# Optimization experiments

Hardware: AMD Instinct MI355X
Metric: run time of the kernel (lower is better)

## Reference

```python
import jax, jax.numpy as jnp
import numpy as np


def _segment_sparsemax(x, batch, B):
    """Per-group sparsemax over a flat ragged tensor.

    x: [N] float values; batch: [N] sorted int group ids in [0, B).
    Groups are contiguous, so an in-group descending sort is a stable
    lexsort on (batch, -x); per-group cumsum is a global cumsum minus the
    cumsum value just before each group's start offset.
    """
    N = x.shape[0]
    num_nodes = jax.ops.segment_sum(jnp.ones(N, jnp.int32), batch, num_segments=B)  # [B]
    start = jnp.concatenate([jnp.zeros(1, jnp.int32), jnp.cumsum(num_nodes)[:-1]])  # [B]

    # shift by per-group max for numerical stability (as in torch forward)
    gmax = jax.ops.segment_max(x, batch, num_segments=B)
    xs = x - gmax[batch]

    # descending sort within each contiguous group
    order = jnp.lexsort((-xs, batch))
    sx = xs[order]  # [N], group-wise descending; group layout unchanged

    # per-group cumulative sum via global cumsum + start offsets
    cs = jnp.cumsum(sx)
    off = jnp.where(start > 0, cs[jnp.maximum(start - 1, 0)], jnp.zeros((), sx.dtype))  # [B]
    seg_cs = cs - off[batch] - 1.0  # input_cumsum - 1.0

    # rho = 1..n_g within each group
    rho = (jnp.arange(N, dtype=jnp.int32) - start[batch] + 1).astype(xs.dtype)

    support = rho * sx > seg_cs  # [N] bool
    supp_size = jax.ops.segment_sum(support.astype(jnp.int32), batch, num_segments=B)  # [B]

    idx = jnp.maximum(supp_size + start - 1, 0)  # [B]
    tau = seg_cs[idx] / supp_size.astype(xs.dtype)  # [B]

    return jnp.maximum(xs - tau[batch], 0.0)


def setup_inputs() -> dict:
    key = jax.random.key(0)
    k1, k2 = jax.random.split(key)
    N = 8_388_608
    B = 4096
    x = jax.random.normal(k1, (N,), dtype=jnp.float32)
    batch = jnp.sort(jax.random.randint(k2, (N,), 0, B)).astype(jnp.int64)
    return {"x": x, "batch": batch, "num_groups": B}


def reference(x, batch, num_groups):
    batch = batch.astype(jnp.int32)
    return _segment_sparsemax(x, batch, int(num_groups))
```

## Files before the change

### kernel.cpp

```cpp
#include <hip/hip_runtime.h>

#define BLK 256
#define QPT 3
#define CAPB (QPT * BLK * 4)
#define CCAP 320


__device__ __forceinline__ float wave_max(float v) {
#pragma unroll
  for (int o = 32; o; o >>= 1) v = fmaxf(v, __shfl_xor(v, o));
  return v;
}
__device__ __forceinline__ float wave_sum(float v) {
#pragma unroll
  for (int o = 32; o; o >>= 1) v += __shfl_xor(v, o);
  return v;
}
__device__ __forceinline__ int wave_sum_i(int v) {
#pragma unroll
  for (int o = 32; o; o >>= 1) v += __shfl_xor(v, o);
  return v;
}

__device__ __forceinline__ void block_sum_cnt(float& s, int& c, float* redf, int* redi, int tid) {
  s = wave_sum(s); c = wave_sum_i(c);
  __syncthreads();
  if ((tid & 63) == 0) { redf[tid >> 6] = s; redi[tid >> 6] = c; }
  __syncthreads();
  s = redf[0] + redf[1] + redf[2] + redf[3];
  c = redi[0] + redi[1] + redi[2] + redi[3];
}

__device__ __forceinline__ int wave_lower_bound(const int* __restrict__ batch, int N,
                                                int target, int lane) {
  int lo = 0, hi = N;
  while (hi > lo) {
    const long long span = hi - lo;
    const int m = lo + (int)((span * (long long)(lane + 1)) / 65);
    const int flag = (batch[m] < target) ? 1 : 0;
    const unsigned long long bal = __ballot(flag);
    const int c = __popcll(bal);
    int nlo = lo, nhi = hi;
    if (c > 0)  nlo = lo + (int)((span * (long long)c) / 65) + 1;
    if (c < 64) nhi = lo + (int)((span * (long long)(c + 1)) / 65);
    lo = nlo; hi = nhi;
  }
  return lo;
}


extern "C" __global__ void __launch_bounds__(BLK)
sparsemax_fused(const float* __restrict__ x, const int* __restrict__ batch,
                const int* __restrict__ pB, float* __restrict__ out, int N) {
  __shared__ float redf[4];
  __shared__ int   redi[4];
  __shared__ float cand[CCAP];
  __shared__ float sorted[64];
  __shared__ int   s_se[2];
  __shared__ int   s_cnt;
  __shared__ float s_csum;
  __shared__ float s_tau;
  const int tid  = threadIdx.x;
  const int lane = tid & 63;
  const int w    = tid >> 6;
  const int B = *pB;

  for (int g = blockIdx.x; g < B; g += gridDim.x) {
    if (w == 0) {
      const int v = wave_lower_bound(batch, N, g, lane);
      if (lane == 0) { s_se[0] = v; s_cnt = 0; s_csum = 0.0f; }
    } else if (w == 1) {
      const int v = wave_lower_bound(batch, N, g + 1, lane);
      if (lane == 0) s_se[1] = v;
    }
    __syncthreads();
    const int s = s_se[0];
    const int e = s_se[1];
    const int n = e - s;
    if (n <= 0) { __syncthreads(); continue; }
    const int a0 = s & ~3;

    if (e - a0 <= CAPB) {
      float4 r[QPT];
      float lmax = -INFINITY;
#pragma unroll
      for (int j = 0; j < QPT; ++j) {
        const int idx = a0 + (j * BLK + tid) * 4;
        float4 v = make_float4(-INFINITY, -INFINITY, -INFINITY, -INFINITY);
        if (idx < e) {
          if (idx + 4 <= N) {
            v = *(const float4*)(x + idx);
          } else {
            if (idx + 0 < N) v.x = x[idx + 0];
            if (idx + 1 < N) v.y = x[idx + 1];
            if (idx + 2 < N) v.z = x[idx + 2];
            if (idx + 3 < N) v.w = x[idx + 3];
          }
          if (idx + 0 < s || idx + 0 >= e) v.x = -INFINITY;
          if (idx + 1 < s || idx + 1 >= e) v.y = -INFINITY;
          if (idx + 2 < s || idx + 2 >= e) v.z = -INFINITY;
          if (idx + 3 < s || idx + 3 >= e) v.w = -INFINITY;
        }
        r[j] = v;
        lmax = fmaxf(lmax, fmaxf(fmaxf(v.x, v.y), fmaxf(v.z, v.w)));
      }
      lmax = wave_max(lmax);
      if (lane == 0) redf[w] = lmax;
      __syncthreads();
      const float gmax = fmaxf(fmaxf(redf[0], redf[1]), fmaxf(redf[2], redf[3]));
      const float thr = gmax - 1.0f;

      float wsum = 0.0f;
#pragma unroll
      for (int j = 0; j < QPT; ++j) {
        const float vv[4] = {r[j].x, r[j].y, r[j].z, r[j].w};
#pragma unroll
        for (int t = 0; t < 4; ++t) {
          const bool p = vv[t] > thr;
          const unsigned long long bal = __ballot(p);
          if (bal) {
            int base = 0;
            if (lane == 0) base = atomicAdd(&s_cnt, __popcll(bal));
            base = __shfl(base, 0);
            if (p) {
              const int off = base + __popcll(bal & ((1ull << lane) - 1ull));
              if (off < CCAP) cand[off] = vv[t];
              wsum += vv[t] - gmax;
            }
          }
        }
      }
      wsum = wave_sum(wsum);
      if (lane == 0) atomicAdd(&s_csum, wsum);
      __syncthreads();
      const int c = s_cnt;

      if (c <= 64) {
        if (w == 0) {
          const float v = (lane < c) ? cand[lane] - gmax : 0.0f;
          int rank = 0;
          for (int q = 0; q < c; ++q) {
            const float t = cand[q] - gmax;
            rank += (t > v) || (t == v && q < lane);
          }
          if (lane < c) sorted[rank] = v;
          const float sv = (lane < c) ? sorted[lane] : 0.0f;
          float cs = sv;
#pragma unroll
          for (int o = 1; o < 64; o <<= 1) {
            const float t2 = __shfl_up(cs, o);
            if (lane >= o) cs += t2;
          }
          const int flag = (lane < c) && (sv * (float)(lane + 1) > cs - 1.0f);
          const unsigned long long bal2 = __ballot(flag);
          const int k = 63 - __clzll(bal2);
          const float csk = __shfl(cs, k);
          if (lane == 0) s_tau = (csk - 1.0f) / (float)(k + 1);
        }
      } else if (c <= CCAP) {
        if (w == 0) {
          float tau = (s_csum - 1.0f) / (float)c;
          int cnt = c;
          for (int it = 0; it < 64; ++it) {
            float s2 = 0.0f; int c2 = 0;
            for (int q = lane; q < c; q += 64) {
              const float vs = cand[q] - gmax;
              if (vs > tau) { s2 += vs; c2++; }
            }
            s2 = wave_sum(s2); c2 = wave_sum_i(c2);
            if (c2 == cnt || c2 == 0) break;
            tau = (s2 - 1.0f) / (float)c2; cnt = c2;
          }
          if (lane == 0) s_tau = tau;
        }
      } else {
        float tau = (s_csum - 1.0f) / (float)c;
        int cnt = c;
        for (int it = 0; it < 64; ++it) {
          float s2 = 0.0f; int c2 = 0;
#pragma unroll
          for (int j = 0; j < QPT; ++j) {
            const float vv[4] = {r[j].x, r[j].y, r[j].z, r[j].w};
#pragma unroll
            for (int t = 0; t < 4; ++t) {
              const float vs = vv[t] - gmax;
              if (vs > tau) { s2 += vs; c2++; }
            }
          }
          block_sum_cnt(s2, c2, redf, redi, tid);
          if (c2 == cnt || c2 == 0) break;
          tau = (s2 - 1.0f) / (float)c2; cnt = c2;
        }
        if (tid == 0) s_tau = tau;
      }
      __syncthreads();
      const float sub = s_tau + gmax;

#pragma unroll
      for (int j = 0; j < QPT; ++j) {
        const int idx = a0 + (j * BLK + tid) * 4;
        if (idx >= e) continue;
        if (idx >= s && idx + 4 <= e) {
          float4 o4;
          o4.x = fmaxf(r[j].x - sub, 0.0f);
          o4.y = fmaxf(r[j].y - sub, 0.0f);
          o4.z = fmaxf(r[j].z - sub, 0.0f);
          o4.w = fmaxf(r[j].w - sub, 0.0f);
          *(float4*)(out + idx) = o4;
        } else {
          const float vv[4] = {r[j].x, r[j].y, r[j].z, r[j].w};
#pragma unroll
          for (int t = 0; t < 4; ++t) {
            const int p2 = idx + t;
            if (p2 >= s && p2 < e) out[p2] = fmaxf(vv[t] - sub, 0.0f);
          }
        }
      }
    } else {
      float gmax = -INFINITY;
      for (int i = s + tid; i < e; i += BLK) gmax = fmaxf(gmax, x[i]);
      gmax = wave_max(gmax);
      if (lane == 0) redf[w] = gmax;
      __syncthreads();
      gmax = fmaxf(fmaxf(redf[0], redf[1]), fmaxf(redf[2], redf[3]));
      float bs = 0.0f; int bc = 0;
      for (int i = s + tid; i < e; i += BLK) {
        const float vs = x[i] - gmax;
        if (vs > -1.0f) { bs += vs; bc++; }
      }
      block_sum_cnt(bs, bc, redf, redi, tid);
      float tau = (bs - 1.0f) / (float)bc;
      int cntS = bc;
      for (int it = 0; it < 64; ++it) {
        float s2 = 0.0f; int c2 = 0;
        for (int i = s + tid; i < e; i += BLK) {
          const float vs = x[i] - gmax;
          if (vs > tau) { s2 += vs; c2++; }
        }
        block_sum_cnt(s2, c2, redf, redi, tid);
        if (c2 == cntS || c2 == 0) break;
        tau = (s2 - 1.0f) / (float)c2; cntS = c2;
      }
      const float sub = tau + gmax;
      for (int i = s + tid; i < e; i += BLK) out[i] = fmaxf(x[i] - sub, 0.0f);
    }
    __syncthreads();
  }
}

extern "C" void kernel_launch(void* const* d_in, const int* in_sizes, int n_in,
                              void* d_out, int out_size, void* d_ws, size_t ws_size,
                              hipStream_t stream) {
  const float* x     = (const float*)d_in[0];
  const int*   batch = (const int*)d_in[1];
  const int*   pB    = (const int*)d_in[2];
  float*       out   = (float*)d_out;
  const int N = in_sizes[0];

  sparsemax_fused<<<dim3(4096), dim3(BLK), 0, stream>>>(x, batch, pB, out, N);
}
```

Measured before the change: 116.0 us.

## Split group boundary search into separate kernel and compact candidates per wave

Moves the per-group binary search over batch ids into a prior kernel that writes a starts array to workspace, so each group block reads its bounds directly instead of running two wave-wide searches followed by a barrier. It also adds a fast path for fully interior float4 loads. Candidate compaction now uses a per-lane count and a wave prefix scan with one atomic per wave, replacing twelve ballot/atomic rounds. The cost is an extra kernel launch and a workspace round trip, and the trailing barrier at the end of each group iteration is removed.

```diff
diff --git a/kernel.cpp b/kernel.cpp
--- a/kernel.cpp
+++ b/kernel.cpp
@@ -50,13 +50,29 @@
 
 
 extern "C" __global__ void __launch_bounds__(BLK)
-sparsemax_fused(const float* __restrict__ x, const int* __restrict__ batch,
-                const int* __restrict__ pB, float* __restrict__ out, int N) {
+build_starts_bs(const int* __restrict__ batch, int* __restrict__ starts,
+                const int* __restrict__ pB, int N) {
+  const int B = *pB;
+  const int lane = threadIdx.x & 63;
+  const int w    = threadIdx.x >> 6;
+  const int wpg  = gridDim.x * (BLK / 64);
+  for (int t = blockIdx.x * (BLK / 64) + w; t <= B; t += wpg) {
+    int v;
+    if (t == 0) v = 0;
+    else if (t >= B) v = N;
+    else v = wave_lower_bound(batch, N, t, lane);
+    if (lane == 0) starts[t] = v;
+  }
+}
+
+
+extern "C" __global__ void __launch_bounds__(BLK)
+sparsemax_groups(const float* __restrict__ x, const int* __restrict__ starts,
+                 const int* __restrict__ pB, float* __restrict__ out, int N) {
   __shared__ float redf[4];
   __shared__ int   redi[4];
   __shared__ float cand[CCAP];
   __shared__ float sorted[64];
-  __shared__ int   s_se[2];
   __shared__ int   s_cnt;
   __shared__ float s_csum;
   __shared__ float s_tau;
@@ -66,18 +82,10 @@
   const int B = *pB;
 
   for (int g = blockIdx.x; g < B; g += gridDim.x) {
-    if (w == 0) {
-      const int v = wave_lower_bound(batch, N, g, lane);
-      if (lane == 0) { s_se[0] = v; s_cnt = 0; s_csum = 0.0f; }
-    } else if (w == 1) {
-      const int v = wave_lower_bound(batch, N, g + 1, lane);
-      if (lane == 0) s_se[1] = v;
-    }
-    __syncthreads();
-    const int s = s_se[0];
-    const int e = s_se[1];
+    const int s = starts[g];
+    const int e = starts[g + 1];
     const int n = e - s;
-    if (n <= 0) { __syncthreads(); continue; }
+    if (n <= 0) continue;
     const int a0 = s & ~3;
 
     if (e - a0 <= CAPB) {
@@ -86,48 +94,61 @@
 #pragma unroll
       for (int j = 0; j < QPT; ++j) {
         const int idx = a0 + (j * BLK + tid) * 4;
-        float4 v = make_float4(-INFINITY, -INFINITY, -INFINITY, -INFINITY);
-        if (idx < e) {
-          if (idx + 4 <= N) {
-            v = *(const float4*)(x + idx);
-          } else {
-            if (idx + 0 < N) v.x = x[idx + 0];
-            if (idx + 1 < N) v.y = x[idx + 1];
-            if (idx + 2 < N) v.z = x[idx + 2];
-            if (idx + 3 < N) v.w = x[idx + 3];
-          }
-          if (idx + 0 < s || idx + 0 >= e) v.x = -INFINITY;
-          if (idx + 1 < s || idx + 1 >= e) v.y = -INFINITY;
-          if (idx + 2 < s || idx + 2 >= e) v.z = -INFINITY;
-          if (idx + 3 < s || idx + 3 >= e) v.w = -INFINITY;
+        float4 v;
+        if (idx >= s && idx + 4 <= e) {
+          v = *(const float4*)(x + idx);
+        } else {
+          v = make_float4(-INFINITY, -INFINITY, -INFINITY, -INFINITY);
+          if (idx < e) {
+            if (idx + 4 <= N) {
+              v = *(const float4*)(x + idx);
+            } else {
+              if (idx + 0 < N) v.x = x[idx + 0];
+              if (idx + 1 < N) v.y = x[idx + 1];
+              if (idx + 2 < N) v.z = x[idx + 2];
+              if (idx + 3 < N) v.w = x[idx + 3];
+            }
+            if (idx + 0 < s || idx + 0 >= e) v.x = -INFINITY;
+            if (idx + 1 < s || idx + 1 >= e) v.y = -INFINITY;
+            if (idx + 2 < s || idx + 2 >= e) v.z = -INFINITY;
+            if (idx + 3 < s || idx + 3 >= e) v.w = -INFINITY;
+          }
         }
         r[j] = v;
         lmax = fmaxf(lmax, fmaxf(fmaxf(v.x, v.y), fmaxf(v.z, v.w)));
       }
       lmax = wave_max(lmax);
       if (lane == 0) redf[w] = lmax;
+      if (tid == 0) { s_cnt = 0; s_csum = 0.0f; }
       __syncthreads();
       const float gmax = fmaxf(fmaxf(redf[0], redf[1]), fmaxf(redf[2], redf[3]));
       const float thr = gmax - 1.0f;
 
-      float wsum = 0.0f;
+      int cm = 0; float wsum = 0.0f;
 #pragma unroll
       for (int j = 0; j < QPT; ++j) {
         const float vv[4] = {r[j].x, r[j].y, r[j].z, r[j].w};
 #pragma unroll
-        for (int t = 0; t < 4; ++t) {
-          const bool p = vv[t] > thr;
-          const unsigned long long bal = __ballot(p);
-          if (bal) {
-            int base = 0;
-            if (lane == 0) base = atomicAdd(&s_cnt, __popcll(bal));
-            base = __shfl(base, 0);
-            if (p) {
-              const int off = base + __popcll(bal & ((1ull << lane) - 1ull));
-              if (off < CCAP) cand[off] = vv[t];
-              wsum += vv[t] - gmax;
-            }
-          }
+        for (int t = 0; t < 4; ++t)
+          if (vv[t] > thr) { cm++; wsum += vv[t] - gmax; }
+      }
+      int pfx = cm;
+#pragma unroll
+      for (int o = 1; o < 64; o <<= 1) {
+        const int t2 = __shfl_up(pfx, o);
+        if (lane >= o) pfx += t2;
+      }
+      int base = 0;
+      if (lane == 63 && pfx > 0) base = atomicAdd(&s_cnt, pfx);
+      base = __shfl(base, 63);
+      int off = base + pfx - cm;
+      if (cm > 0) {
+#pragma unroll
+        for (int j = 0; j < QPT; ++j) {
+          const float vv[4] = {r[j].x, r[j].y, r[j].z, r[j].w};
+#pragma unroll
+          for (int t = 0; t < 4; ++t)
+            if (vv[t] > thr) { if (off < CCAP) cand[off] = vv[t]; off++; }
         }
       }
       wsum = wave_sum(wsum);
@@ -244,7 +265,6 @@
       const float sub = tau + gmax;
       for (int i = s + tid; i < e; i += BLK) out[i] = fmaxf(x[i] - sub, 0.0f);
     }
-    __syncthreads();
   }
 }
 
@@ -257,5 +277,8 @@
   float*       out   = (float*)d_out;
   const int N = in_sizes[0];
 
-  sparsemax_fused<<<dim3(4096), dim3(BLK), 0, stream>>>(x, batch, pB, out, N);
-}
+  int* starts = (int*)d_ws;
+
+  build_starts_bs<<<dim3(1025), dim3(BLK), 0, stream>>>(batch, starts, pB, N);
+  sparsemax_groups<<<dim3(4096), dim3(BLK), 0, stream>>>(x, starts, pB, out, N);
+}
```

Result: no change. 114.1 us (-1.7%).
